# Optimization experiments

Hardware: AMD Instinct MI355X
Metric: run time of the kernel (lower is better)

The kernel has to match this reference:

```python
import jax, jax.numpy as jnp
import numpy as np

DIM_H = 384
EPS = 0.5
HID = 768
NN = 3   # num_normal_labels (B,I,O)
NL = 7   # num_labels (O, B/I x POS/NEG/NEU)


def _make_w_trans():
    # ote_vocab: B=0, I=1, O=2 ; ts_vocab: O=0, B-POS=1, B-NEG=2, B-NEU=3, I-POS=4, I-NEG=5, I-NEU=6
    W = np.zeros((NN, NL), dtype=np.float32)
    W[0, 1] = W[0, 2] = W[0, 3] = 1.0 / 3.0  # B -> B-*
    W[1, 4] = W[1, 5] = W[1, 6] = 1.0 / 3.0  # I -> I-*
    W[2, 0] = 1.0                            # O -> O
    return jnp.asarray(W)


def setup_inputs() -> dict:
    key = jax.random.key(0)
    ks = jax.random.split(key, 16)
    B, S = 32, 512
    s = 0.02
    inp = {
        'x': jax.random.normal(ks[0], (B, S, HID), jnp.float32),
        'attention_mask': jnp.ones((B, S), jnp.int32),
        'labels': jax.random.randint(ks[1], (B, S), 0, NL, jnp.int32),
        'labels_normal': jax.random.randint(ks[2], (B, S), 0, NN, jnp.int32),
        'W_fc_normal': jax.random.normal(ks[3], (HID, NN), jnp.float32) * s,
        'b_fc_normal': jnp.zeros((NN,), jnp.float32),
        'w_ih_f': jax.random.normal(ks[4], (4 * DIM_H, HID), jnp.float32) * s,
        'w_hh_f': jax.random.normal(ks[5], (4 * DIM_H, DIM_H), jnp.float32) * s,
        'b_f': jnp.zeros((4 * DIM_H,), jnp.float32),
        'w_ih_b': jax.random.normal(ks[6], (4 * DIM_H, HID), jnp.float32) * s,
        'w_hh_b': jax.random.normal(ks[7], (4 * DIM_H, DIM_H), jnp.float32) * s,
        'b_b': jnp.zeros((4 * DIM_H,), jnp.float32),
        'W_gate': jax.random.uniform(ks[8], (2 * DIM_H, 2 * DIM_H), jnp.float32, -0.2, 0.2),
        'W_fc_upper': jax.random.normal(ks[9], (2 * DIM_H, NL), jnp.float32) * s,
        'b_fc_upper': jnp.zeros((NL,), jnp.float32),
        'W_trans': _make_w_trans(),
    }
    return inp


def _lstm_dir(xs, w_ih, w_hh, b):
    # xs: [S, B, HID] time-major; PyTorch gate order i,f,g,o
    B = xs.shape[1]
    pre = jnp.einsum('sbh,gh->sbg', xs, w_ih) + b  # precompute input projections

    def step(carry, p_t):
        h, c = carry
        g = p_t + h @ w_hh.T
        i, f, gg, o = jnp.split(g, 4, axis=-1)
        c = jax.nn.sigmoid(f) * c + jax.nn.sigmoid(i) * jnp.tanh(gg)
        h = jax.nn.sigmoid(o) * jnp.tanh(c)
        return (h, c), h

    init = (jnp.zeros((B, DIM_H), xs.dtype), jnp.zeros((B, DIM_H), xs.dtype))
    _, hs = jax.lax.scan(step, init, pre)
    return hs  # [S, B, DIM_H]


def _masked_ce(logits, labels, mask):
    logp = jax.nn.log_softmax(logits, axis=-1)
    nll = -jnp.take_along_axis(logp, labels[..., None].astype(jnp.int32), axis=-1)[..., 0]
    m = mask.astype(logits.dtype)
    return jnp.sum(nll * m) / jnp.sum(m)


def reference(x, attention_mask, labels, labels_normal, W_fc_normal, b_fc_normal,
              w_ih_f, w_hh_f, b_f, w_ih_b, w_hh_b, b_b, W_gate,
              W_fc_upper, b_fc_upper, W_trans):
    z_t = x @ W_fc_normal + b_fc_normal                      # [B,S,NN]
    loss = _masked_ce(z_t, labels_normal, attention_mask)

    xs = jnp.transpose(x, (1, 0, 2))                         # [S,B,HID]
    hf = _lstm_dir(xs, w_ih_f, w_hh_f, b_f)
    hb = _lstm_dir(xs[::-1], w_ih_b, w_hh_b, b_b)[::-1]
    h_s = jnp.concatenate([hf, hb], axis=-1)                 # [S,B,2*DIM_H]

    # gated highway recurrence: gates depend only on h_s -> batched matmul + linear scan
    g = jax.nn.sigmoid(h_s @ W_gate)                         # [S,B,768]

    def gate_step(h_prev, inp):
        ht, gt = inp
        h = gt * ht + (1.0 - gt) * h_prev
        return h, h

    _, rest = jax.lax.scan(gate_step, h_s[0], (h_s[1:], g[1:]))
    h_tilde = jnp.concatenate([h_s[:1], rest], axis=0)       # [S,B,768]
    h_tilde = jnp.transpose(h_tilde, (1, 0, 2))              # [B,S,768]; dropout = identity (eval)

    z_s = h_tilde @ W_fc_upper + b_fc_upper                  # [B,S,NL]
    p = jax.nn.softmax(z_t, axis=-1)
    alpha = EPS * jnp.sum(p * p, axis=-1, keepdims=True)     # [B,S,1]
    z_s_prime = z_t @ W_trans                                # [B,S,NL]
    z_s_tilde = z_s_prime * alpha + z_s * (1.0 - alpha)

    loss = loss + _masked_ce(z_s_tilde, labels, attention_mask)
    return loss, z_s_tilde
```

## Files before the change

### kernel.cpp

```cpp
#include <hip/hip_runtime.h>

#define B_SZ   32
#define S_LEN  512
#define HID    768
#define DH     384
#define G4     1536
#define NPOS   16384
#define EPS_C  0.5f
#define NCH    24576
#define CHK    64
#define NCHK   8

typedef _Float16 h2 __attribute__((ext_vector_type(2)));
typedef short bf16x8 __attribute__((ext_vector_type(8)));
typedef float f32x4 __attribute__((ext_vector_type(4)));

static __device__ __forceinline__ float sigm(float x) { return 1.0f / (1.0f + __expf(-x)); }

static __device__ __forceinline__ unsigned short f2bf(float f) {
    union { float f; unsigned u; } v; v.f = f;
    unsigned r = v.u + 0x7FFF + ((v.u >> 16) & 1);
    return (unsigned short)(r >> 16);
}
static __device__ __forceinline__ float bf2f(unsigned short u) {
    union { unsigned u; float f; } v; v.u = ((unsigned)u) << 16; return v.f;
}

static __device__ __forceinline__ float wred(float v) {
#pragma unroll
    for (int off = 32; off > 0; off >>= 1) v += __shfl_down(v, off, 64);
    return v;
}

static __device__ __forceinline__ float dot2acc(h2 a, h2 b, float c) {
#if __has_builtin(__builtin_amdgcn_fdot2)
    return __builtin_amdgcn_fdot2(a, b, c, false);
#else
    return c + (float)a.x * (float)b.x + (float)a.y * (float)b.y;
#endif
}

__global__ void wprep(const float* __restrict__ wf, const float* __restrict__ wb,
                      unsigned* __restrict__ wpk) {
    int gid = blockIdx.x * 256 + threadIdx.x;
    int d = (gid >= 294912) ? 1 : 0;
    int j = gid - d * 294912;
    const float* src = d ? wb : wf;
    _Float16 a = (_Float16)src[2 * j];
    _Float16 b = (_Float16)src[2 * j + 1];
    unsigned pa = __builtin_bit_cast(unsigned short, a);
    unsigned pb = __builtin_bit_cast(unsigned short, b);
    wpk[(size_t)d * 294912 + j] = pa | (pb << 16);
}

__global__ __launch_bounds__(256) void cast_bf16(
    const float* __restrict__ src, unsigned short* __restrict__ dst, int n4) {
    int i = blockIdx.x * 256 + threadIdx.x;
    if (i >= n4) return;
    float4 v = *(const float4*)(src + (size_t)i * 4);
    ushort4 o;
    o.x = f2bf(v.x); o.y = f2bf(v.y); o.z = f2bf(v.z); o.w = f2bf(v.w);
    *(ushort4*)(dst + (size_t)i * 4) = o;
}

__global__ __launch_bounds__(256) void wgt_prep(
    const float* __restrict__ Wg, unsigned short* __restrict__ Wgt) {
    int i = blockIdx.x * 256 + threadIdx.x;
    int k = i / 768, n = i - k * 768;
    Wgt[(size_t)n * 768 + k] = f2bf(Wg[i]);
}

__global__ __launch_bounds__(256) void zt_kernel(
    const float* __restrict__ x, const int* __restrict__ amask,
    const int* __restrict__ labn, const float* __restrict__ Wfc,
    const float* __restrict__ bfc, const float* __restrict__ Wtr,
    float* __restrict__ alpha, float* __restrict__ zsp,
    float* __restrict__ p0, float* __restrict__ p2) {
    const int gid  = blockIdx.x * blockDim.x + threadIdx.x;
    const int pos  = gid >> 6, lane = gid & 63, wv = threadIdx.x >> 6;
    __shared__ float r0[4], r2[4];
    const float* xp = x + (size_t)pos * HID;
    float a0 = 0.f, a1 = 0.f, a2 = 0.f;
#pragma unroll
    for (int j = 0; j < 12; ++j) {
        int k = lane + (j << 6);
        float xv = xp[k];
        a0 += xv * Wfc[k * 3 + 0];
        a1 += xv * Wfc[k * 3 + 1];
        a2 += xv * Wfc[k * 3 + 2];
    }
    a0 = wred(a0); a1 = wred(a1); a2 = wred(a2);
    if (lane == 0) {
        float z0 = a0 + bfc[0], z1 = a1 + bfc[1], z2 = a2 + bfc[2];
        float mx = fmaxf(z0, fmaxf(z1, z2));
        float e0 = __expf(z0 - mx), e1 = __expf(z1 - mx), e2 = __expf(z2 - mx);
        float se = e0 + e1 + e2;
        float m  = (float)amask[pos];
        int  lab = labn[pos];
        float zl = (lab == 0) ? z0 : ((lab == 1) ? z1 : z2);
        r0[wv] = (mx + __logf(se) - zl) * m;
        r2[wv] = m;
        float q0 = e0 / se, q1 = e1 / se, q2 = e2 / se;
        alpha[pos] = EPS_C * (q0 * q0 + q1 * q1 + q2 * q2);
#pragma unroll
        for (int cc = 0; cc < 7; ++cc)
            zsp[(size_t)pos * 7 + cc] = z0 * Wtr[cc] + z1 * Wtr[7 + cc] + z2 * Wtr[14 + cc];
    }
    __syncthreads();
    if (threadIdx.x == 0) {
        p0[blockIdx.x] = r0[0] + r0[1] + r0[2] + r0[3];
        p2[blockIdx.x] = r2[0] + r2[1] + r2[2] + r2[3];
    }
}

__global__ __launch_bounds__(256) void gemm_mfma(
    const unsigned short* __restrict__ A, const unsigned short* __restrict__ B,
    const float* __restrict__ bias, void* __restrict__ Cout,
    int M, int N, int K, int mode) {
    __shared__ __align__(16) unsigned short As[128][40];
    __shared__ __align__(16) unsigned short Bs[128][40];
    const int tid = threadIdx.x;
    const int m0 = blockIdx.y * 128, n0 = blockIdx.x * 128;
    const int wave = tid >> 6, lane = tid & 63;
    const int wm = (wave & 1) * 64, wn = (wave >> 1) * 64;
    const int lm = lane & 15, quad = lane >> 4;
    f32x4 acc[4][4] = {};

    for (int k0 = 0; k0 < K; k0 += 32) {
#pragma unroll
        for (int r = 0; r < 2; ++r) {
            int seg = tid + r * 256;
            int row = seg >> 2, c16 = (seg & 3) << 3;
            uint4 va = *(const uint4*)(A + (size_t)(m0 + row) * K + k0 + c16);
            *(uint4*)&As[row][c16] = va;
            uint4 vb = *(const uint4*)(B + (size_t)(n0 + row) * K + k0 + c16);
            *(uint4*)&Bs[row][c16] = vb;
        }
        __syncthreads();
        bf16x8 af[4], bfr[4];
#pragma unroll
        for (int i = 0; i < 4; ++i) {
            af[i]  = *(const bf16x8*)&As[wm + i * 16 + lm][quad * 8];
            bfr[i] = *(const bf16x8*)&Bs[wn + i * 16 + lm][quad * 8];
        }
#pragma unroll
        for (int mi = 0; mi < 4; ++mi)
#pragma unroll
            for (int ni = 0; ni < 4; ++ni)
                acc[mi][ni] = __builtin_amdgcn_mfma_f32_16x16x32_bf16(
                    af[mi], bfr[ni], acc[mi][ni], 0, 0, 0);
        __syncthreads();
    }

    const int rbase = quad * 4;
#pragma unroll
    for (int mi = 0; mi < 4; ++mi) {
#pragma unroll
        for (int ni = 0; ni < 4; ++ni) {
            const int col = n0 + wn + ni * 16 + lm;
            const float bv = (mode == 0) ? bias[col] : 0.0f;
#pragma unroll
            for (int r = 0; r < 4; ++r) {
                const int row = m0 + wm + mi * 16 + rbase + r;
                float v = acc[mi][ni][r];
                if (mode == 0)
                    ((unsigned short*)Cout)[(size_t)row * N + col] = f2bf(v + bv);
                else
                    ((float*)Cout)[(size_t)row * N + col] = sigm(v);
            }
        }
    }
}

#define WLOAD(i) const uint4 wr##i = wq[i];
#define WDOT(i) \
    a0 = dot2acc(__builtin_bit_cast(h2, wr##i.x), hp[4*(i)+0], a0); \
    a1 = dot2acc(__builtin_bit_cast(h2, wr##i.y), hp[4*(i)+1], a1); \
    a2 = dot2acc(__builtin_bit_cast(h2, wr##i.z), hp[4*(i)+2], a2); \
    a3 = dot2acc(__builtin_bit_cast(h2, wr##i.w), hp[4*(i)+3], a3);

__global__ __launch_bounds__(768) void lstm_scan3(
    const unsigned* __restrict__ wpk,
    const unsigned short* __restrict__ pre,
    float* __restrict__ h_s,
    unsigned short* __restrict__ h_sb,
    unsigned long long* __restrict__ hx64) {
    const int blk   = blockIdx.x;
    const int chain = blk & 63;
    const int bp    = blk >> 6;
    const int d = chain >> 5, b = chain & 31;
    const int tid = threadIdx.x;
    const int r = tid >> 1, p = tid & 1;
    const int g = r / 96;
    const int u = r - g * 96;
    const int base = bp * 96;
    const int G = g * 384 + base + u;

    __shared__ __align__(16) _Float16 lh16[384];
    __shared__ float lpre[384];

    const uint4* wq = (const uint4*)(wpk + ((size_t)d * 1536 + G) * 192 + p * 96);
    WLOAD(0)  WLOAD(1)  WLOAD(2)  WLOAD(3)  WLOAD(4)  WLOAD(5)
    WLOAD(6)  WLOAD(7)  WLOAD(8)  WLOAD(9)  WLOAD(10) WLOAD(11)
    WLOAD(12) WLOAD(13) WLOAD(14) WLOAD(15) WLOAD(16) WLOAD(17)
    WLOAD(18) WLOAD(19) WLOAD(20) WLOAD(21) WLOAD(22) WLOAD(23)

    const unsigned short* prb = pre + ((size_t)d * B_SZ + b) * S_LEN * G4;
    float c = 0.0f;

    for (int s = 0; s < S_LEN; ++s) {
        const int t = d ? (S_LEN - 1 - s) : s;
        float prev = bf2f(prb[(size_t)t * G4 + G]);

        if (s == 0) {
            if (tid < 384) lh16[tid] = (_Float16)0.0f;
        } else if (tid < 288) {
            const int uu = tid + (tid >= base ? 96 : 0);
            const unsigned long long* srcp =
                hx64 + ((size_t)((s - 1) & 1) * 64 + chain) * 384 + uu;
            unsigned long long v =
                __hip_atomic_load(srcp, __ATOMIC_RELAXED, __HIP_MEMORY_SCOPE_AGENT);
            while ((unsigned)(v >> 32) != (unsigned)(s - 1)) {
                __builtin_amdgcn_s_sleep(1);
                v = __hip_atomic_load(srcp, __ATOMIC_RELAXED, __HIP_MEMORY_SCOPE_AGENT);
            }
            lh16[uu] = (_Float16)__builtin_bit_cast(float, (unsigned)v);
        }
        __syncthreads();

        {
            const h2* hp = ((const h2*)lh16) + p * 96;
            float a0 = (p == 0) ? prev : 0.0f, a1 = 0.f, a2 = 0.f, a3 = 0.f;
            WDOT(0)  WDOT(1)  WDOT(2)  WDOT(3)  WDOT(4)  WDOT(5)
            WDOT(6)  WDOT(7)  WDOT(8)  WDOT(9)  WDOT(10) WDOT(11)
            WDOT(12) WDOT(13) WDOT(14) WDOT(15) WDOT(16) WDOT(17)
            WDOT(18) WDOT(19) WDOT(20) WDOT(21) WDOT(22) WDOT(23)
            float acc = (a0 + a1) + (a2 + a3);
            lpre[r] = acc + __shfl_xor(acc, 1, 64);
        }
        __syncthreads();

        if (tid < 96) {
            float gi = lpre[tid], gf = lpre[96 + tid], gg = lpre[192 + tid], go = lpre[288 + tid];
            c = sigm(gf) * c + sigm(gi) * tanhf(gg);
            float h = sigm(go) * tanhf(c);
            const size_t oidx = ((size_t)t * B_SZ + b) * HID + d * DH + base + tid;
            h_s[oidx]  = h;
            h_sb[oidx] = f2bf(h);
            lh16[base + tid] = (_Float16)h;
            unsigned long long v = ((unsigned long long)(unsigned)s << 32)
                                 | (unsigned long long)__builtin_bit_cast(unsigned, h);
            __hip_atomic_store(hx64 + ((size_t)(s & 1) * 64 + chain) * 384 + base + tid,
                               v, __ATOMIC_RELAXED, __HIP_MEMORY_SCOPE_AGENT);
        }
    }
}

__global__ __launch_bounds__(256) void gscanA(
    const float* __restrict__ g, const float* __restrict__ hs,
    float2* __restrict__ ab) {
    int id = blockIdx.x * 256 + threadIdx.x;
    int chunk = id / NCH, chain = id - chunk * NCH;
    int t0 = chunk * CHK;
    float A = 1.f, Bv = 0.f;
    for (int i = 0; i < CHK; ++i) {
        int t = t0 + i;
        size_t idx = (size_t)t * NCH + chain;
        float gv = g[idx];
        float hv = hs[idx];
        float a = (t == 0) ? 0.f : (1.f - gv);
        float bb = (t == 0) ? hv : gv * hv;
        A  = a * A;
        Bv = a * Bv + bb;
    }
    ab[id] = make_float2(A, Bv);
}

__global__ __launch_bounds__(256) void gscanB(
    const float2* __restrict__ ab, float* __restrict__ cin) {
    int chain = blockIdx.x * 256 + threadIdx.x;
    float h = 0.f;
#pragma unroll
    for (int j = 0; j < NCHK; ++j) {
        cin[(size_t)j * NCH + chain] = h;
        float2 t = ab[(size_t)j * NCH + chain];
        h = t.x * h + t.y;
    }
}

__global__ __launch_bounds__(256) void gscanC(
    const float* __restrict__ g, float* __restrict__ hs,
    const float* __restrict__ cin) {
    int id = blockIdx.x * 256 + threadIdx.x;
    int chunk = id / NCH, chain = id - chunk * NCH;
    int t0 = chunk * CHK;
    float h = cin[(size_t)chunk * NCH + chain];
    for (int i = 0; i < CHK; ++i) {
        int t = t0 + i;
        size_t idx = (size_t)t * NCH + chain;
        float gv = g[idx];
        float v  = hs[idx];
        h = (t == 0) ? v : (gv * v + (1.f - gv) * h);
        hs[idx] = h;
    }
}

__global__ __launch_bounds__(256) void final_k(
    const float* __restrict__ ht, const float* __restrict__ Wup,
    const float* __restrict__ bup, const float* __restrict__ alpha,
    const float* __restrict__ zsp, const int* __restrict__ labels,
    const int* __restrict__ amask, float* __restrict__ out, float* __restrict__ p1) {
    const int gid = blockIdx.x * blockDim.x + threadIdx.x;
    const int pos = gid >> 6, lane = gid & 63, wv = threadIdx.x >> 6;
    __shared__ float r1[4];
    const int bb = pos >> 9, tt = pos & 511;
    const float* hp = ht + (size_t)tt * (B_SZ * HID) + (size_t)bb * HID;
    float acc[7] = {};
#pragma unroll
    for (int j = 0; j < 12; ++j) {
        int k = lane + (j << 6);
        float hv = hp[k];
        const float* wr = Wup + k * 7;
#pragma unroll
        for (int cc = 0; cc < 7; ++cc) acc[cc] += hv * wr[cc];
    }
#pragma unroll
    for (int cc = 0; cc < 7; ++cc) acc[cc] = wred(acc[cc]);
    if (lane == 0) {
        float al = alpha[pos];
        float z[7], mx = -1e30f;
#pragma unroll
        for (int cc = 0; cc < 7; ++cc) {
            float v = acc[cc] + bup[cc];
            v = zsp[(size_t)pos * 7 + cc] * al + v * (1.0f - al);
            z[cc] = v;
            mx = fmaxf(mx, v);
            out[1 + (size_t)pos * 7 + cc] = v;
        }
        float se = 0.f;
#pragma unroll
        for (int cc = 0; cc < 7; ++cc) se += __expf(z[cc] - mx);
        float lse = mx + __logf(se);
        int lab = labels[pos];
        float zl = z[0];
#pragma unroll
        for (int cc = 1; cc < 7; ++cc) if (lab == cc) zl = z[cc];
        float m = (float)amask[pos];
        r1[wv] = (lse - zl) * m;
    }
    __syncthreads();
    if (threadIdx.x == 0)
        p1[blockIdx.x] = r1[0] + r1[1] + r1[2] + r1[3];
}

__global__ __launch_bounds__(256) void loss_k(
    const float* __restrict__ p0, const float* __restrict__ p1,
    const float* __restrict__ p2, float* __restrict__ out) {
    const int tid = threadIdx.x, lane = tid & 63, wv = tid >> 6;
    __shared__ float rs[4][3];
    float s0 = 0.f, s1 = 0.f, s2 = 0.f;
    for (int i = tid; i < 4096; i += 256) {
        s0 += p0[i]; s1 += p1[i]; s2 += p2[i];
    }
    s0 = wred(s0); s1 = wred(s1); s2 = wred(s2);
    if (lane == 0) { rs[wv][0] = s0; rs[wv][1] = s1; rs[wv][2] = s2; }
    __syncthreads();
    if (tid == 0) {
        float t0 = rs[0][0] + rs[1][0] + rs[2][0] + rs[3][0];
        float t1 = rs[0][1] + rs[1][1] + rs[2][1] + rs[3][1];
        float t2 = rs[0][2] + rs[1][2] + rs[2][2] + rs[3][2];
        out[0] = t0 / t2 + t1 / t2;
    }
}

extern "C" void kernel_launch(void* const* d_in, const int* in_sizes, int n_in,
                              void* d_out, int out_size, void* d_ws, size_t ws_size,
                              hipStream_t stream) {
    const float* x     = (const float*)d_in[0];
    const int*   amask = (const int*)d_in[1];
    const int*   labels= (const int*)d_in[2];
    const int*   labn  = (const int*)d_in[3];
    const float* Wfc   = (const float*)d_in[4];
    const float* bfc   = (const float*)d_in[5];
    const float* wihf  = (const float*)d_in[6];
    const float* whhf  = (const float*)d_in[7];
    const float* bf    = (const float*)d_in[8];
    const float* wihb  = (const float*)d_in[9];
    const float* whhb  = (const float*)d_in[10];
    const float* bb    = (const float*)d_in[11];
    const float* Wg    = (const float*)d_in[12];
    const float* Wup   = (const float*)d_in[13];
    const float* bup   = (const float*)d_in[14];
    const float* Wtr   = (const float*)d_in[15];
    float* out = (float*)d_out;
    (void)in_sizes; (void)n_in; (void)out_size; (void)ws_size;

    char* ws = (char*)d_ws;
    size_t off = 0;
    auto alloc = [&](size_t bytes) -> char* {
        char* p = ws + off;
        off = (off + bytes + 255) & ~(size_t)255;
        return p;
    };
    unsigned* w16buf    = (unsigned*)alloc((size_t)2 * 1536 * 192 * 4);
    unsigned short* pre = (unsigned short*)alloc((size_t)2 * NPOS * G4 * 2);
    float* hs           = (float*)alloc((size_t)NPOS * HID * 4);
    unsigned short* xb  = (unsigned short*)alloc((size_t)NPOS * HID * 2);
    unsigned short* wfb = (unsigned short*)alloc((size_t)G4 * HID * 2);
    unsigned short* wbb = (unsigned short*)alloc((size_t)G4 * HID * 2);
    unsigned short* wgt = (unsigned short*)alloc((size_t)HID * HID * 2);
    float* alpha        = (float*)alloc((size_t)NPOS * 4);
    float* zsp          = (float*)alloc((size_t)NPOS * 7 * 4);
    unsigned long long* hx64 = (unsigned long long*)alloc((size_t)2 * 64 * 384 * 8);
    float2* ab          = (float2*)alloc((size_t)NCHK * NCH * 8);
    float* cin          = (float*)alloc((size_t)NCHK * NCH * 4);
    float* part0        = (float*)alloc(4096 * 4);
    float* part1        = (float*)alloc(4096 * 4);
    float* part2        = (float*)alloc(4096 * 4);
    float* gbuf          = (float*)pre;
    unsigned short* h_sb = xb;


    wprep<<<2304, 256, 0, stream>>>(whhf, whhb, w16buf);
    cast_bf16<<<12288, 256, 0, stream>>>(x, xb, NPOS * HID / 4);
    cast_bf16<<<1152, 256, 0, stream>>>(wihf, wfb, G4 * HID / 4);
    cast_bf16<<<1152, 256, 0, stream>>>(wihb, wbb, G4 * HID / 4);
    wgt_prep<<<2304, 256, 0, stream>>>(Wg, wgt);

    zt_kernel<<<4096, 256, 0, stream>>>(x, amask, labn, Wfc, bfc, Wtr, alpha, zsp,
                                        part0, part2);

    gemm_mfma<<<dim3(12, 128), 256, 0, stream>>>(xb, wfb, bf, pre, NPOS, G4, HID, 0);
    gemm_mfma<<<dim3(12, 128), 256, 0, stream>>>(xb, wbb, bb, pre + (size_t)NPOS * G4,
                                                 NPOS, G4, HID, 0);

    lstm_scan3<<<256, 768, 0, stream>>>(w16buf, pre, hs, h_sb, hx64);

    gemm_mfma<<<dim3(6, 128), 256, 0, stream>>>(h_sb, wgt, nullptr, gbuf, NPOS, HID, HID, 1);

    gscanA<<<768, 256, 0, stream>>>(gbuf, hs, ab);
    gscanB<<<96, 256, 0, stream>>>(ab, cin);
    gscanC<<<768, 256, 0, stream>>>(gbuf, hs, cin);

    final_k<<<4096, 256, 0, stream>>>(hs, Wup, bup, alpha, zsp, labels, amask, out, part1);

    loss_k<<<1, 256, 0, stream>>>(part0, part1, part2, out);
}
```

Baseline: 1.371 ms.

## Replace per-chain LSTM recurrence with batched MFMA across batch per direction

The recurrent LSTM kernel is restructured from 256 blocks (one chain per batch/direction split across 4 unit groups using fp16 dot2) into 64 blocks, where each block owns 12 hidden units for all 32 batch elements of one direction. The recurrent matvec becomes a small bf16 MFMA GEMM, with weights held in registers and h staged in double-buffered LDS. Cross-block exchange of h goes through a global publish buffer using sequence-tagged atomics, and tanh is replaced with an exp-based approximation. This cuts per-step launch width and makes better use of the matrix units, but each block now has to gather h from 31 other blocks every step, and the recurrent weights drop from fp16 to bf16 precision.

Measured after the change: 5.151 ms. 3.76x slower.

```diff
diff --git a/kernel.cpp b/kernel.cpp
--- a/kernel.cpp
+++ b/kernel.cpp
@@ -10,12 +10,16 @@
 #define NCH    24576
 #define CHK    64
 #define NCHK   8
-
-typedef _Float16 h2 __attribute__((ext_vector_type(2)));
+#define UPB    12
+#define GPD    32
+
 typedef short bf16x8 __attribute__((ext_vector_type(8)));
 typedef float f32x4 __attribute__((ext_vector_type(4)));
 
 static __device__ __forceinline__ float sigm(float x) { return 1.0f / (1.0f + __expf(-x)); }
+static __device__ __forceinline__ float tanh_fast(float x) {
+    return 1.0f - 2.0f / (__expf(2.0f * x) + 1.0f);
+}
 
 static __device__ __forceinline__ unsigned short f2bf(float f) {
     union { float f; unsigned u; } v; v.f = f;
@@ -30,27 +34,6 @@
 #pragma unroll
     for (int off = 32; off > 0; off >>= 1) v += __shfl_down(v, off, 64);
     return v;
-}
-
-static __device__ __forceinline__ float dot2acc(h2 a, h2 b, float c) {
-#if __has_builtin(__builtin_amdgcn_fdot2)
-    return __builtin_amdgcn_fdot2(a, b, c, false);
-#else
-    return c + (float)a.x * (float)b.x + (float)a.y * (float)b.y;
-#endif
-}
-
-__global__ void wprep(const float* __restrict__ wf, const float* __restrict__ wb,
-                      unsigned* __restrict__ wpk) {
-    int gid = blockIdx.x * 256 + threadIdx.x;
-    int d = (gid >= 294912) ? 1 : 0;
-    int j = gid - d * 294912;
-    const float* src = d ? wb : wf;
-    _Float16 a = (_Float16)src[2 * j];
-    _Float16 b = (_Float16)src[2 * j + 1];
-    unsigned pa = __builtin_bit_cast(unsigned short, a);
-    unsigned pb = __builtin_bit_cast(unsigned short, b);
-    wpk[(size_t)d * 294912 + j] = pa | (pb << 16);
 }
 
 __global__ __launch_bounds__(256) void cast_bf16(
@@ -172,86 +155,107 @@
     }
 }
 
-#define WLOAD(i) const uint4 wr##i = wq[i];
-#define WDOT(i) \
-    a0 = dot2acc(__builtin_bit_cast(h2, wr##i.x), hp[4*(i)+0], a0); \
-    a1 = dot2acc(__builtin_bit_cast(h2, wr##i.y), hp[4*(i)+1], a1); \
-    a2 = dot2acc(__builtin_bit_cast(h2, wr##i.z), hp[4*(i)+2], a2); \
-    a3 = dot2acc(__builtin_bit_cast(h2, wr##i.w), hp[4*(i)+3], a3);
-
-__global__ __launch_bounds__(768) void lstm_scan3(
-    const unsigned* __restrict__ wpk,
+__global__ __launch_bounds__(384, 1) void lstm_mfma(
+    const unsigned short* __restrict__ whb,
     const unsigned short* __restrict__ pre,
     float* __restrict__ h_s,
     unsigned short* __restrict__ h_sb,
-    unsigned long long* __restrict__ hx64) {
-    const int blk   = blockIdx.x;
-    const int chain = blk & 63;
-    const int bp    = blk >> 6;
-    const int d = chain >> 5, b = chain & 31;
+    unsigned long long* __restrict__ hpub) {
+    const int blk = blockIdx.x;
+    const int d = blk >> 5, gblk = blk & 31, u0 = gblk * UPB;
     const int tid = threadIdx.x;
-    const int r = tid >> 1, p = tid & 1;
-    const int g = r / 96;
-    const int u = r - g * 96;
-    const int base = bp * 96;
-    const int G = g * 384 + base + u;
-
-    __shared__ __align__(16) _Float16 lh16[384];
-    __shared__ float lpre[384];
-
-    const uint4* wq = (const uint4*)(wpk + ((size_t)d * 1536 + G) * 192 + p * 96);
-    WLOAD(0)  WLOAD(1)  WLOAD(2)  WLOAD(3)  WLOAD(4)  WLOAD(5)
-    WLOAD(6)  WLOAD(7)  WLOAD(8)  WLOAD(9)  WLOAD(10) WLOAD(11)
-    WLOAD(12) WLOAD(13) WLOAD(14) WLOAD(15) WLOAD(16) WLOAD(17)
-    WLOAD(18) WLOAD(19) WLOAD(20) WLOAD(21) WLOAD(22) WLOAD(23)
-
-    const unsigned short* prb = pre + ((size_t)d * B_SZ + b) * S_LEN * G4;
+    const int wave = tid >> 6, lane = tid & 63;
+    const int lm = lane & 15, quad = lane >> 4;
+    const int mt = wave >> 1, nt = wave & 1;
+    const int su = tid % UPB, sb = tid / UPB;
+
+    __shared__ __align__(16) unsigned short Ht[2][32][392];
+    __shared__ __align__(16) float preT[32][52];
+
+    bf16x8 afr[12];
+    {
+        const int lr = mt * 16 + lm;
+        const int gate = lr / UPB, uu = lr - gate * UPB;
+        const unsigned short* wr =
+            whb + ((size_t)d * G4 + gate * 384 + u0 + uu) * 384;
+#pragma unroll
+        for (int kt = 0; kt < 12; ++kt)
+            afr[kt] = *(const bf16x8*)(wr + kt * 32 + quad * 8);
+    }
+
     float c = 0.0f;
+    const unsigned short* prb = pre + ((size_t)d * B_SZ + sb) * S_LEN * G4;
 
     for (int s = 0; s < S_LEN; ++s) {
         const int t = d ? (S_LEN - 1 - s) : s;
-        float prev = bf2f(prb[(size_t)t * G4 + G]);
+        const int par = s & 1;
+
+        const unsigned short* pp = prb + (size_t)t * G4 + u0 + su;
+        const float pi = bf2f(pp[0]);
+        const float pf = bf2f(pp[384]);
+        const float pg = bf2f(pp[768]);
+        const float po = bf2f(pp[1152]);
 
         if (s == 0) {
-            if (tid < 384) lh16[tid] = (_Float16)0.0f;
-        } else if (tid < 288) {
-            const int uu = tid + (tid >= base ? 96 : 0);
-            const unsigned long long* srcp =
-                hx64 + ((size_t)((s - 1) & 1) * 64 + chain) * 384 + uu;
-            unsigned long long v =
-                __hip_atomic_load(srcp, __ATOMIC_RELAXED, __HIP_MEMORY_SCOPE_AGENT);
-            while ((unsigned)(v >> 32) != (unsigned)(s - 1)) {
-                __builtin_amdgcn_s_sleep(1);
-                v = __hip_atomic_load(srcp, __ATOMIC_RELAXED, __HIP_MEMORY_SCOPE_AGENT);
+            for (int i = tid; i < 32 * 196; i += 384)
+                ((unsigned*)&Ht[0][0][0])[i] = 0;
+        } else {
+            const unsigned long long* pb = hpub + ((size_t)(par * 2 + d)) * 384 * 32;
+            unsigned long long v[31];
+#pragma unroll
+            for (int i = 0; i < 31; ++i) {
+                const int e = i * 384 + tid;
+                const int rk = e >> 5, b = e & 31;
+                const int k = rk + (rk >= u0 ? UPB : 0);
+                v[i] = __hip_atomic_load(pb + (size_t)k * 32 + b,
+                                         __ATOMIC_RELAXED, __HIP_MEMORY_SCOPE_AGENT);
             }
-            lh16[uu] = (_Float16)__builtin_bit_cast(float, (unsigned)v);
+#pragma unroll
+            for (int i = 0; i < 31; ++i) {
+                const int e = i * 384 + tid;
+                const int rk = e >> 5, b = e & 31;
+                const int k = rk + (rk >= u0 ? UPB : 0);
+                while ((unsigned)(v[i] >> 32) != (unsigned)s) {
+                    __builtin_amdgcn_s_sleep(1);
+                    v[i] = __hip_atomic_load(pb + (size_t)k * 32 + b,
+                                             __ATOMIC_RELAXED, __HIP_MEMORY_SCOPE_AGENT);
+                }
+                Ht[par][b][k] = f2bf(__builtin_bit_cast(float, (unsigned)v[i]));
+            }
         }
         __syncthreads();
 
         {
-            const h2* hp = ((const h2*)lh16) + p * 96;
-            float a0 = (p == 0) ? prev : 0.0f, a1 = 0.f, a2 = 0.f, a3 = 0.f;
-            WDOT(0)  WDOT(1)  WDOT(2)  WDOT(3)  WDOT(4)  WDOT(5)
-            WDOT(6)  WDOT(7)  WDOT(8)  WDOT(9)  WDOT(10) WDOT(11)
-            WDOT(12) WDOT(13) WDOT(14) WDOT(15) WDOT(16) WDOT(17)
-            WDOT(18) WDOT(19) WDOT(20) WDOT(21) WDOT(22) WDOT(23)
-            float acc = (a0 + a1) + (a2 + a3);
-            lpre[r] = acc + __shfl_xor(acc, 1, 64);
+            f32x4 a0 = {}, a1 = {};
+#pragma unroll
+            for (int kt = 0; kt < 12; kt += 2) {
+                bf16x8 b0 = *(const bf16x8*)&Ht[par][nt * 16 + lm][kt * 32 + quad * 8];
+                bf16x8 b1 = *(const bf16x8*)&Ht[par][nt * 16 + lm][(kt + 1) * 32 + quad * 8];
+                a0 = __builtin_amdgcn_mfma_f32_16x16x32_bf16(afr[kt],     b0, a0, 0, 0, 0);
+                a1 = __builtin_amdgcn_mfma_f32_16x16x32_bf16(afr[kt + 1], b1, a1, 0, 0, 0);
+            }
+            f32x4 acc = a0 + a1;
+            *(f32x4*)&preT[nt * 16 + lm][mt * 16 + quad * 4] = acc;
         }
         __syncthreads();
 
-        if (tid < 96) {
-            float gi = lpre[tid], gf = lpre[96 + tid], gg = lpre[192 + tid], go = lpre[288 + tid];
-            c = sigm(gf) * c + sigm(gi) * tanhf(gg);
-            float h = sigm(go) * tanhf(c);
-            const size_t oidx = ((size_t)t * B_SZ + b) * HID + d * DH + base + tid;
-            h_s[oidx]  = h;
-            h_sb[oidx] = f2bf(h);
-            lh16[base + tid] = (_Float16)h;
-            unsigned long long v = ((unsigned long long)(unsigned)s << 32)
-                                 | (unsigned long long)__builtin_bit_cast(unsigned, h);
-            __hip_atomic_store(hx64 + ((size_t)(s & 1) * 64 + chain) * 384 + base + tid,
-                               v, __ATOMIC_RELAXED, __HIP_MEMORY_SCOPE_AGENT);
+        {
+            float gi = preT[sb][su]           + pi;
+            float gf = preT[sb][UPB + su]     + pf;
+            float gg = preT[sb][2 * UPB + su] + pg;
+            float go = preT[sb][3 * UPB + su] + po;
+            c = sigm(gf) * c + sigm(gi) * tanh_fast(gg);
+            float h = sigm(go) * tanh_fast(c);
+            const size_t oidx = ((size_t)t * B_SZ + sb) * HID + d * DH + u0 + su;
+            h_s[oidx] = h;
+            unsigned short hb = f2bf(h);
+            h_sb[oidx] = hb;
+            Ht[par ^ 1][sb][u0 + su] = hb;
+            unsigned long long pv = ((unsigned long long)(unsigned)(s + 1) << 32)
+                                  | (unsigned long long)__builtin_bit_cast(unsigned, h);
+            __hip_atomic_store(hpub + ((size_t)(((par ^ 1) * 2 + d)) * 384
+                                       + (u0 + su)) * 32 + sb,
+                               pv, __ATOMIC_RELAXED, __HIP_MEMORY_SCOPE_AGENT);
         }
     }
 }
@@ -402,7 +406,7 @@
         off = (off + bytes + 255) & ~(size_t)255;
         return p;
     };
-    unsigned* w16buf    = (unsigned*)alloc((size_t)2 * 1536 * 192 * 4);
+    unsigned short* whb = (unsigned short*)alloc((size_t)2 * G4 * 384 * 2);
     unsigned short* pre = (unsigned short*)alloc((size_t)2 * NPOS * G4 * 2);
     float* hs           = (float*)alloc((size_t)NPOS * HID * 4);
     unsigned short* xb  = (unsigned short*)alloc((size_t)NPOS * HID * 2);
@@ -411,7 +415,7 @@
     unsigned short* wgt = (unsigned short*)alloc((size_t)HID * HID * 2);
     float* alpha        = (float*)alloc((size_t)NPOS * 4);
     float* zsp          = (float*)alloc((size_t)NPOS * 7 * 4);
-    unsigned long long* hx64 = (unsigned long long*)alloc((size_t)2 * 64 * 384 * 8);
+    unsigned long long* hpub = (unsigned long long*)alloc((size_t)2 * 2 * 384 * 32 * 8);
     float2* ab          = (float2*)alloc((size_t)NCHK * NCH * 8);
     float* cin          = (float*)alloc((size_t)NCHK * NCH * 4);
     float* part0        = (float*)alloc(4096 * 4);
@@ -421,7 +425,8 @@
     unsigned short* h_sb = xb;
 
 
-    wprep<<<2304, 256, 0, stream>>>(whhf, whhb, w16buf);
+    cast_bf16<<<576, 256, 0, stream>>>(whhf, whb, G4 * 384 / 4);
+    cast_bf16<<<576, 256, 0, stream>>>(whhb, whb + (size_t)G4 * 384, G4 * 384 / 4);
     cast_bf16<<<12288, 256, 0, stream>>>(x, xb, NPOS * HID / 4);
     cast_bf16<<<1152, 256, 0, stream>>>(wihf, wfb, G4 * HID / 4);
     cast_bf16<<<1152, 256, 0, stream>>>(wihb, wbb, G4 * HID / 4);
@@ -434,7 +439,7 @@
     gemm_mfma<<<dim3(12, 128), 256, 0, stream>>>(xb, wbb, bb, pre + (size_t)NPOS * G4,
                                                  NPOS, G4, HID, 0);
 
-    lstm_scan3<<<256, 768, 0, stream>>>(w16buf, pre, hs, h_sb, hx64);
+    lstm_mfma<<<64, 384, 0, stream>>>(whb, pre, hs, h_sb, hpub);
 
     gemm_mfma<<<dim3(6, 128), 256, 0, stream>>>(h_sb, wgt, nullptr, gbuf, NPOS, HID, HID, 1);
 
```
